# Optimization experiments

Hardware: AMD Instinct MI355X
Metric: run time of the kernel (lower is better)

## Reference

```python
import jax, jax.numpy as jnp
import numpy as np

DILATIONS = (1, 4, 16)

def setup_inputs() -> dict:
    key = jax.random.key(0)
    k1, _ = jax.random.split(key)
    B, C, H, W = 4, 64, 512, 512
    u = jax.random.normal(k1, (B, C, H, W), dtype=jnp.float32)
    # matches nn.Parameter(torch.ones(len(dilations), channels) * 0.1)
    D = jnp.full((len(DILATIONS), C), 0.1, dtype=jnp.float32)
    return {"u": u, "D": D}

def _lap5(u, d):
    # 5-point stencil at dilation d with replicate (edge) boundary:
    # u(x+d,y)+u(x-d,y)+u(x,y+d)+u(x,y-d)-4u(x,y)
    p = jnp.pad(u, ((0, 0), (0, 0), (d, d), (d, d)), mode='edge')
    H, W = u.shape[-2], u.shape[-1]
    up    = p[:, :, :H,     d:d+W]
    down  = p[:, :, 2*d:,   d:d+W]
    left  = p[:, :, d:d+H,  :W]
    right = p[:, :, d:d+H,  2*d:]
    return up + down + left + right - 4.0 * u

def reference(u, D):
    out = jnp.zeros_like(u)
    for i, d in enumerate(DILATIONS):
        scale = jax.nn.softplus(D[i])[None, :, None, None]  # (1,C,1,1)
        out = out + scale * _lap5(u, d)
    return out
```

## Files before the change

### kernel.cpp

```cpp
#include <hip/hip_runtime.h>
#include <math.h>

#define HH 512
#define WW 512
#define W4Q 128
#define IMG (HH * WW)
#define NR 64
#define RST 129
#define SS 32
#define HALF 256

typedef float f32x4 __attribute__((ext_vector_type(4)));

__device__ __forceinline__ f32x4 bc4(float v) { f32x4 r = {v, v, v, v}; return r; }
__device__ __forceinline__ float softplus(float x) {
    return fmaxf(x, 0.0f) + log1pf(expf(-fabsf(x)));
}

__global__ __launch_bounds__(512, 2) void lap3_kernel(const float* __restrict__ u,
                                                      const float* __restrict__ D,
                                                      float* __restrict__ out) {
    __shared__ f32x4 lds[NR * RST];

    const int b    = blockIdx.x;
    const int bc   = b >> 1;
    const int row0 = (b & 1) * HALF;
    const int c    = bc & 63;

    const float s0 = softplus(D[c]);
    const float s1 = softplus(D[64 + c]);
    const float s2 = softplus(D[128 + c]);
    const float m4c = -4.0f * (s0 + s1 + s2);

    const int t  = threadIdx.x;
    const int q  = t & 127;
    const int g  = t >> 7;
    const int sc = t & 15;
    const int sr = t >> 4;

    const f32x4* __restrict__ img4 =
        reinterpret_cast<const f32x4*>(u) + (size_t)bc * (IMG / 4);
    f32x4* __restrict__ out4 =
        reinterpret_cast<f32x4*>(out) + (size_t)bc * (IMG / 4);

#pragma unroll
    for (int rnd = 0; rnd < 2; ++rnd) {
        const int vrow = row0 - 16 + rnd * 32 + sr;
        const int crow = min(max(vrow, 0), HH - 1);
        const int slot = vrow & (NR - 1);
#pragma unroll
        for (int j = 0; j < 8; ++j) {
            const int qc = sc + 16 * j;
            lds[slot * RST + qc] = img4[crow * W4Q + qc];
        }
    }
    __syncthreads();

    const int qm1 = max(q - 1, 0), qp1 = min(q + 1, W4Q - 1);
    const int qm4 = max(q - 4, 0), qp4 = min(q + 4, W4Q - 1);
    const bool pl4 = (q == 0), pr4 = (q == W4Q - 1);
    const bool pl16 = (q < 4), pr16 = (q > W4Q - 5);

#pragma unroll 1
    for (int step = 0; step < HALF / SS; ++step) {
        const int h0 = row0 + step * SS;

        f32x4 gbuf[8];
        int nslot = 0;
        const bool do_stage = (step + 1 < HALF / SS);
        if (do_stage) {
            const int vrow = h0 + 48 + sr;
            const int crow = min(vrow, HH - 1);
            nslot = vrow & (NR - 1);
#pragma unroll
            for (int j = 0; j < 8; ++j)
                gbuf[j] = img4[crow * W4Q + sc + 16 * j];
        }

        const int hr = h0 + g * 8;
        f32x4 C[10];
#pragma unroll
        for (int k = 0; k < 10; ++k)
            C[k] = lds[((hr - 1 + k) & (NR - 1)) * RST + q];
        f32x4 U4[3], D4v[3];
#pragma unroll
        for (int k = 0; k < 3; ++k)
            U4[k] = lds[((hr - 4 + k) & (NR - 1)) * RST + q];
#pragma unroll
        for (int k = 0; k < 3; ++k)
            D4v[k] = lds[((hr + 9 + k) & (NR - 1)) * RST + q];

#pragma unroll
        for (int r = 0; r < 8; ++r) {
            const int rs = ((hr + r) & (NR - 1)) * RST;
            f32x4 l4 = lds[rs + qm1];  if (pl4)  l4 = bc4(l4.x);
            f32x4 r4 = lds[rs + qp1];  if (pr4)  r4 = bc4(r4.w);
            f32x4 l16 = lds[rs + qm4]; if (pl16) l16 = bc4(l16.x);
            f32x4 r16 = lds[rs + qp4]; if (pr16) r16 = bc4(r16.w);
            const f32x4 u16 = lds[((hr + r - 16) & (NR - 1)) * RST + q];
            const f32x4 d16 = lds[((hr + r + 16) & (NR - 1)) * RST + q];

            const f32x4 cc = C[r + 1], up1 = C[r], dn1 = C[r + 2];
            const f32x4 u4 = (r < 3) ? U4[r] : C[r - 3];
            const f32x4 d4 = (r > 4) ? D4v[r - 5] : C[r + 5];

            f32x4 l1 = { l4.w, cc.x, cc.y, cc.z };
            f32x4 r1 = { cc.y, cc.z, cc.w, r4.x };

            const f32x4 d1s  = (up1 + dn1) + (l1 + r1);
            const f32x4 d4s  = (u4 + d4) + (l4 + r4);
            const f32x4 d16s = (u16 + d16) + (l16 + r16);

            f32x4 o;
#pragma unroll
            for (int j = 0; j < 4; ++j) {
                float acc = m4c * cc[j];
                acc = fmaf(s0, d1s[j], acc);
                acc = fmaf(s1, d4s[j], acc);
                acc = fmaf(s2, d16s[j], acc);
                o[j] = acc;
            }
            __builtin_nontemporal_store(o, out4 + (hr + r) * W4Q + q);
        }

        __syncthreads();
        if (do_stage) {
#pragma unroll
            for (int j = 0; j < 8; ++j)
                lds[nslot * RST + sc + 16 * j] = gbuf[j];
        }
        __syncthreads();
    }
}

extern "C" void kernel_launch(void* const* d_in, const int* in_sizes, int n_in,
                              void* d_out, int out_size, void* d_ws, size_t ws_size,
                              hipStream_t stream) {
    const float* u = (const float*)d_in[0];
    const float* D = (const float*)d_in[1];
    float* out = (float*)d_out;

    lap3_kernel<<<512, 512, 0, stream>>>(u, D, out);
}
```

Baseline: 87.75 us.

## Split each image half into column strips with halo for smaller blocks

Each (batch, channel, half) tile is now split into four 32-quad column strips, each with a 4-quad halo on either side. Edge-replicate padding is applied when the halo is staged into LDS. This shrinks per-block LDS from about 132KB to 42KB and launches 2048 blocks of 256 threads instead of 512 blocks of 512, aiming for better occupancy and load balance across CUs. The cost is roughly 25% extra global reads for the halo columns, which should mostly hit in cache, plus per-element index division during staging.

```diff
diff --git a/kernel.cpp b/kernel.cpp
--- a/kernel.cpp
+++ b/kernel.cpp
@@ -2,13 +2,13 @@
 #include <math.h>
 
 #define HH 512
-#define WW 512
 #define W4Q 128
-#define IMG (HH * WW)
+#define IMG (HH * 512)
 #define NR 64
-#define RST 129
+#define RST 41
 #define SS 32
 #define HALF 256
+#define NSTEP (HALF / SS)
 
 typedef float f32x4 __attribute__((ext_vector_type(4)));
 
@@ -17,15 +17,17 @@
     return fmaxf(x, 0.0f) + log1pf(expf(-fabsf(x)));
 }
 
-__global__ __launch_bounds__(512, 2) void lap3_kernel(const float* __restrict__ u,
+__global__ __launch_bounds__(256, 3) void lap3_kernel(const float* __restrict__ u,
                                                       const float* __restrict__ D,
                                                       float* __restrict__ out) {
     __shared__ f32x4 lds[NR * RST];
 
-    const int b    = blockIdx.x;
-    const int bc   = b >> 1;
-    const int row0 = (b & 1) * HALF;
+    const int bid  = blockIdx.x;
+    const int bc   = bid >> 3;
+    const int cq   = bid & 3;
+    const int row0 = ((bid >> 2) & 1) * HALF;
     const int c    = bc & 63;
+    const int gq0  = cq * 32;
 
     const float s0 = softplus(D[c]);
     const float s1 = softplus(D[64 + c]);
@@ -33,79 +35,91 @@
     const float m4c = -4.0f * (s0 + s1 + s2);
 
     const int t  = threadIdx.x;
-    const int q  = t & 127;
-    const int g  = t >> 7;
-    const int sc = t & 15;
-    const int sr = t >> 4;
+    const int q  = t & 31;
+    const int g  = t >> 5;
+    const int wq = q + 4;
 
     const f32x4* __restrict__ img4 =
         reinterpret_cast<const f32x4*>(u) + (size_t)bc * (IMG / 4);
     f32x4* __restrict__ out4 =
         reinterpret_cast<f32x4*>(out) + (size_t)bc * (IMG / 4);
 
+    auto stage_now = [&](int vrow0) {
 #pragma unroll
-    for (int rnd = 0; rnd < 2; ++rnd) {
-        const int vrow = row0 - 16 + rnd * 32 + sr;
-        const int crow = min(max(vrow, 0), HH - 1);
-        const int slot = vrow & (NR - 1);
-#pragma unroll
-        for (int j = 0; j < 8; ++j) {
-            const int qc = sc + 16 * j;
-            lds[slot * RST + qc] = img4[crow * W4Q + qc];
+        for (int j = 0; j < 5; ++j) {
+            const int idx = j * 256 + t;
+            const int rr  = idx / 40;
+            const int col = idx - rr * 40;
+            const int vrow = vrow0 + rr;
+            const int crow = min(max(vrow, 0), HH - 1);
+            const int vgq  = gq0 - 4 + col;
+            const int gqc  = min(max(vgq, 0), W4Q - 1);
+            f32x4 v = img4[crow * W4Q + gqc];
+            if (vgq < 0)       v = bc4(v.x);
+            if (vgq > W4Q - 1) v = bc4(v.w);
+            lds[(vrow & (NR - 1)) * RST + col] = v;
         }
-    }
+    };
+
+    stage_now(row0 - 16);
+    stage_now(row0 + 16);
     __syncthreads();
 
-    const int qm1 = max(q - 1, 0), qp1 = min(q + 1, W4Q - 1);
-    const int qm4 = max(q - 4, 0), qp4 = min(q + 4, W4Q - 1);
-    const bool pl4 = (q == 0), pr4 = (q == W4Q - 1);
-    const bool pl16 = (q < 4), pr16 = (q > W4Q - 5);
+#pragma unroll 1
+    for (int step = 0; step < NSTEP; ++step) {
+        const int h0 = row0 + step * SS;
+        const bool do_stage = (step < NSTEP - 1);
 
-#pragma unroll 1
-    for (int step = 0; step < HALF / SS; ++step) {
-        const int h0 = row0 + step * SS;
-
-        f32x4 gbuf[8];
-        int nslot = 0;
-        const bool do_stage = (step + 1 < HALF / SS);
+        f32x4 gbuf[5];
+        int gaddr[5];
         if (do_stage) {
-            const int vrow = h0 + 48 + sr;
-            const int crow = min(vrow, HH - 1);
-            nslot = vrow & (NR - 1);
+            const int vrow0 = h0 + 48;
 #pragma unroll
-            for (int j = 0; j < 8; ++j)
-                gbuf[j] = img4[crow * W4Q + sc + 16 * j];
+            for (int j = 0; j < 5; ++j) {
+                const int idx = j * 256 + t;
+                const int rr  = idx / 40;
+                const int col = idx - rr * 40;
+                const int vrow = vrow0 + rr;
+                const int crow = min(vrow, HH - 1);
+                const int vgq  = gq0 - 4 + col;
+                const int gqc  = min(max(vgq, 0), W4Q - 1);
+                f32x4 v = img4[crow * W4Q + gqc];
+                if (vgq < 0)       v = bc4(v.x);
+                if (vgq > W4Q - 1) v = bc4(v.w);
+                gbuf[j] = v;
+                gaddr[j] = (vrow & (NR - 1)) * RST + col;
+            }
         }
 
-        const int hr = h0 + g * 8;
-        f32x4 C[10];
+        const int hr = h0 + g * 4;
+        f32x4 C[6];
 #pragma unroll
-        for (int k = 0; k < 10; ++k)
-            C[k] = lds[((hr - 1 + k) & (NR - 1)) * RST + q];
+        for (int k = 0; k < 6; ++k)
+            C[k] = lds[((hr - 1 + k) & (NR - 1)) * RST + wq];
         f32x4 U4[3], D4v[3];
 #pragma unroll
         for (int k = 0; k < 3; ++k)
-            U4[k] = lds[((hr - 4 + k) & (NR - 1)) * RST + q];
+            U4[k] = lds[((hr - 4 + k) & (NR - 1)) * RST + wq];
 #pragma unroll
         for (int k = 0; k < 3; ++k)
-            D4v[k] = lds[((hr + 9 + k) & (NR - 1)) * RST + q];
+            D4v[k] = lds[((hr + 5 + k) & (NR - 1)) * RST + wq];
 
 #pragma unroll
-        for (int r = 0; r < 8; ++r) {
+        for (int r = 0; r < 4; ++r) {
             const int rs = ((hr + r) & (NR - 1)) * RST;
-            f32x4 l4 = lds[rs + qm1];  if (pl4)  l4 = bc4(l4.x);
-            f32x4 r4 = lds[rs + qp1];  if (pr4)  r4 = bc4(r4.w);
-            f32x4 l16 = lds[rs + qm4]; if (pl16) l16 = bc4(l16.x);
-            f32x4 r16 = lds[rs + qp4]; if (pr16) r16 = bc4(r16.w);
-            const f32x4 u16 = lds[((hr + r - 16) & (NR - 1)) * RST + q];
-            const f32x4 d16 = lds[((hr + r + 16) & (NR - 1)) * RST + q];
+            const f32x4 l4  = lds[rs + wq - 1];
+            const f32x4 r4  = lds[rs + wq + 1];
+            const f32x4 l16 = lds[rs + wq - 4];
+            const f32x4 r16 = lds[rs + wq + 4];
+            const f32x4 u16 = lds[((hr + r - 16) & (NR - 1)) * RST + wq];
+            const f32x4 d16 = lds[((hr + r + 16) & (NR - 1)) * RST + wq];
 
             const f32x4 cc = C[r + 1], up1 = C[r], dn1 = C[r + 2];
-            const f32x4 u4 = (r < 3) ? U4[r] : C[r - 3];
-            const f32x4 d4 = (r > 4) ? D4v[r - 5] : C[r + 5];
+            const f32x4 u4 = (r < 3) ? U4[r] : C[0];
+            const f32x4 d4 = (r == 0) ? C[5] : D4v[r - 1];
 
-            f32x4 l1 = { l4.w, cc.x, cc.y, cc.z };
-            f32x4 r1 = { cc.y, cc.z, cc.w, r4.x };
+            const f32x4 l1 = { l4.w, cc.x, cc.y, cc.z };
+            const f32x4 r1 = { cc.y, cc.z, cc.w, r4.x };
 
             const f32x4 d1s  = (up1 + dn1) + (l1 + r1);
             const f32x4 d4s  = (u4 + d4) + (l4 + r4);
@@ -120,14 +134,14 @@
                 acc = fmaf(s2, d16s[j], acc);
                 o[j] = acc;
             }
-            __builtin_nontemporal_store(o, out4 + (hr + r) * W4Q + q);
+            __builtin_nontemporal_store(o, out4 + (hr + r) * W4Q + gq0 + q);
         }
 
         __syncthreads();
         if (do_stage) {
 #pragma unroll
-            for (int j = 0; j < 8; ++j)
-                lds[nslot * RST + sc + 16 * j] = gbuf[j];
+            for (int j = 0; j < 5; ++j)
+                lds[gaddr[j]] = gbuf[j];
         }
         __syncthreads();
     }
@@ -140,5 +154,5 @@
     const float* D = (const float*)d_in[1];
     float* out = (float*)d_out;
 
-    lap3_kernel<<<512, 512, 0, stream>>>(u, D, out);
+    lap3_kernel<<<2048, 256, 0, stream>>>(u, D, out);
 }
```

Measured after the change: 103.6 us. 18.1% more time.

## Halve stencil step size, stage full rows per wave, drop one barrier

Applied to the files above, without the earlier changes.

Each loop step now covers 16 rows instead of 32, so each thread computes 4 output rows and prefetches 4 staging rows. Each group of 128 threads now loads whole rows, for both the initial fill and the per-step staging. The barrier before the LDS staging write is removed, which is safe because the slots being overwritten belong to rows the current step does not read. The `__launch_bounds__(512, 2)` minimum-blocks hint is dropped. These changes aim to cut register pressure and barrier stalls, at the cost of more loop iterations and more halo reloads from LDS per output row.

```diff
diff --git a/kernel.cpp b/kernel.cpp
--- a/kernel.cpp
+++ b/kernel.cpp
@@ -2,13 +2,13 @@
 #include <math.h>
 
 #define HH 512
-#define WW 512
 #define W4Q 128
-#define IMG (HH * WW)
+#define IMG (HH * 512)
 #define NR 64
 #define RST 129
-#define SS 32
+#define SS 16
 #define HALF 256
+#define NSTEP (HALF / SS)
 
 typedef float f32x4 __attribute__((ext_vector_type(4)));
 
@@ -17,9 +17,9 @@
     return fmaxf(x, 0.0f) + log1pf(expf(-fabsf(x)));
 }
 
-__global__ __launch_bounds__(512, 2) void lap3_kernel(const float* __restrict__ u,
-                                                      const float* __restrict__ D,
-                                                      float* __restrict__ out) {
+__global__ __launch_bounds__(512) void lap3_kernel(const float* __restrict__ u,
+                                                   const float* __restrict__ D,
+                                                   float* __restrict__ out) {
     __shared__ f32x4 lds[NR * RST];
 
     const int b    = blockIdx.x;
@@ -35,8 +35,7 @@
     const int t  = threadIdx.x;
     const int q  = t & 127;
     const int g  = t >> 7;
-    const int sc = t & 15;
-    const int sr = t >> 4;
+    const int sr = t >> 7;
 
     const f32x4* __restrict__ img4 =
         reinterpret_cast<const f32x4*>(u) + (size_t)bc * (IMG / 4);
@@ -44,15 +43,10 @@
         reinterpret_cast<f32x4*>(out) + (size_t)bc * (IMG / 4);
 
 #pragma unroll
-    for (int rnd = 0; rnd < 2; ++rnd) {
-        const int vrow = row0 - 16 + rnd * 32 + sr;
+    for (int j = 0; j < 12; ++j) {
+        const int vrow = row0 - 16 + sr + 4 * j;
         const int crow = min(max(vrow, 0), HH - 1);
-        const int slot = vrow & (NR - 1);
-#pragma unroll
-        for (int j = 0; j < 8; ++j) {
-            const int qc = sc + 16 * j;
-            lds[slot * RST + qc] = img4[crow * W4Q + qc];
-        }
+        lds[(vrow & (NR - 1)) * RST + q] = img4[crow * W4Q + q];
     }
     __syncthreads();
 
@@ -62,25 +56,24 @@
     const bool pl16 = (q < 4), pr16 = (q > W4Q - 5);
 
 #pragma unroll 1
-    for (int step = 0; step < HALF / SS; ++step) {
+    for (int step = 0; step < NSTEP; ++step) {
         const int h0 = row0 + step * SS;
+        const bool do_stage = (step < NSTEP - 1);
 
-        f32x4 gbuf[8];
-        int nslot = 0;
-        const bool do_stage = (step + 1 < HALF / SS);
+        f32x4 gbuf[4];
         if (do_stage) {
-            const int vrow = h0 + 48 + sr;
-            const int crow = min(vrow, HH - 1);
-            nslot = vrow & (NR - 1);
 #pragma unroll
-            for (int j = 0; j < 8; ++j)
-                gbuf[j] = img4[crow * W4Q + sc + 16 * j];
+            for (int j = 0; j < 4; ++j) {
+                const int vrow = h0 + 32 + sr + 4 * j;
+                const int crow = min(vrow, HH - 1);
+                gbuf[j] = img4[crow * W4Q + q];
+            }
         }
 
-        const int hr = h0 + g * 8;
-        f32x4 C[10];
+        const int hr = h0 + g * 4;
+        f32x4 C[6];
 #pragma unroll
-        for (int k = 0; k < 10; ++k)
+        for (int k = 0; k < 6; ++k)
             C[k] = lds[((hr - 1 + k) & (NR - 1)) * RST + q];
         f32x4 U4[3], D4v[3];
 #pragma unroll
@@ -88,10 +81,10 @@
             U4[k] = lds[((hr - 4 + k) & (NR - 1)) * RST + q];
 #pragma unroll
         for (int k = 0; k < 3; ++k)
-            D4v[k] = lds[((hr + 9 + k) & (NR - 1)) * RST + q];
+            D4v[k] = lds[((hr + 5 + k) & (NR - 1)) * RST + q];
 
 #pragma unroll
-        for (int r = 0; r < 8; ++r) {
+        for (int r = 0; r < 4; ++r) {
             const int rs = ((hr + r) & (NR - 1)) * RST;
             f32x4 l4 = lds[rs + qm1];  if (pl4)  l4 = bc4(l4.x);
             f32x4 r4 = lds[rs + qp1];  if (pr4)  r4 = bc4(r4.w);
@@ -101,11 +94,11 @@
             const f32x4 d16 = lds[((hr + r + 16) & (NR - 1)) * RST + q];
 
             const f32x4 cc = C[r + 1], up1 = C[r], dn1 = C[r + 2];
-            const f32x4 u4 = (r < 3) ? U4[r] : C[r - 3];
-            const f32x4 d4 = (r > 4) ? D4v[r - 5] : C[r + 5];
+            const f32x4 u4 = (r < 3) ? U4[r] : C[0];
+            const f32x4 d4 = (r == 0) ? C[5] : D4v[r - 1];
 
-            f32x4 l1 = { l4.w, cc.x, cc.y, cc.z };
-            f32x4 r1 = { cc.y, cc.z, cc.w, r4.x };
+            const f32x4 l1 = { l4.w, cc.x, cc.y, cc.z };
+            const f32x4 r1 = { cc.y, cc.z, cc.w, r4.x };
 
             const f32x4 d1s  = (up1 + dn1) + (l1 + r1);
             const f32x4 d4s  = (u4 + d4) + (l4 + r4);
@@ -123,11 +116,12 @@
             __builtin_nontemporal_store(o, out4 + (hr + r) * W4Q + q);
         }
 
-        __syncthreads();
         if (do_stage) {
 #pragma unroll
-            for (int j = 0; j < 8; ++j)
-                lds[nslot * RST + sc + 16 * j] = gbuf[j];
+            for (int j = 0; j < 4; ++j) {
+                const int vrow = h0 + 32 + sr + 4 * j;
+                lds[(vrow & (NR - 1)) * RST + q] = gbuf[j];
+            }
         }
         __syncthreads();
     }
```

Result: no change. 86.92 us (-0.9%).
